# Optimization experiments

Measured on AMD Instinct MI355X. Metric: run time of the kernel, lower is better.

Reference implementation:

```python
import jax, jax.numpy as jnp
import numpy as np

B, L, LOCAL_DIM, M = 4096, 256, 2, 64

def setup_inputs() -> dict:
    key = jax.random.key(0)
    k1, k2 = jax.random.split(key)
    samples = jax.random.randint(k1, (B, L), 0, LOCAL_DIM, dtype=jnp.int32)
    # epsilon near 1 so the product over L=256 sites is numerically stable
    epsilon = 1.0 + 0.05 * jax.random.normal(k2, (LOCAL_DIM, M, L), dtype=jnp.float32)
    return {"samples": samples, "epsilon": epsilon}

def reference(samples, epsilon):
    # samples: (B, L) int occupancies in [0, local_dim)
    # epsilon: (local_dim, M, L)
    # qGPS full path with no_syms: out[b] = sum_m prod_l epsilon[samples[b,l], m, l]
    Ls = samples.shape[-1]
    eps_t = jnp.transpose(epsilon, (2, 0, 1))          # (L, local_dim, M)
    gathered = eps_t[jnp.arange(Ls)[None, :], samples]  # (B, L, M) gather by occupancy
    site_prod = jnp.prod(gathered, axis=1)              # (B, M) product over sites
    return jnp.sum(site_prod, axis=-1)                  # (B,) sum over support dim M
```

## Files before the change

kernel.cpp:

```cpp
#include <hip/hip_runtime.h>

#define LQ 256
#define MQ 64
#define SW 264

typedef __attribute__((ext_vector_type(8))) short bf16x8;
typedef __attribute__((ext_vector_type(4))) float f32x4;

#if defined(__has_builtin) && __has_builtin(__builtin_amdgcn_logf)
#define LOG2F(x) __builtin_amdgcn_logf(x)
#else
#define LOG2F(x) __log2f(x)
#endif
#if defined(__has_builtin) && __has_builtin(__builtin_amdgcn_exp2f)
#define EXP2F(x) __builtin_amdgcn_exp2f(x)
#else
#define EXP2F(x) exp2f(x)
#endif

__device__ __forceinline__ unsigned short f2bf(float x) {
    unsigned u = __float_as_uint(x);
    u += 0x7FFFu + ((u >> 16) & 1u);
    return (unsigned short)(u >> 16);
}

__global__ __launch_bounds__(256) void qgps_mfma(const int* __restrict__ samples,
                                                 const float* __restrict__ eps,
                                                 float* __restrict__ out) {
    __shared__ __attribute__((aligned(16))) unsigned short Wt[MQ * SW];
    __shared__ __attribute__((aligned(16))) unsigned short St[16 * SW];
    __shared__ float bred[MQ * 4];
    __shared__ float red[4][16];

    const int tid = threadIdx.x;
    const int w = tid >> 6;
    const int lane = tid & 63;
    const int b0 = blockIdx.x * 16;

    {
        const int m = tid >> 2;
        const int ls = (tid & 3) * 64;
        const float4* e0v = (const float4*)(eps + m * LQ + ls);
        const float4* e1v = (const float4*)(eps + MQ * LQ + m * LQ + ls);
        unsigned short* wrow = &Wt[m * SW + ls];
        float acc0 = 0.f;
#pragma unroll
        for (int i = 0; i < 16; ++i) {
            float4 a = e0v[i], c = e1v[i];
            float l0 = LOG2F(a.x), l1 = LOG2F(a.y);
            float l2 = LOG2F(a.z), l3 = LOG2F(a.w);
            acc0 += (l0 + l1) + (l2 + l3);
            ushort2 p0 = make_ushort2(f2bf(LOG2F(c.x) - l0), f2bf(LOG2F(c.y) - l1));
            ushort2 p1 = make_ushort2(f2bf(LOG2F(c.z) - l2), f2bf(LOG2F(c.w) - l3));
            *(ushort2*)&wrow[4 * i] = p0;
            *(ushort2*)&wrow[4 * i + 2] = p1;
        }
        bred[m * 4 + (tid & 3)] = acc0;
    }

    {
        const int bl = tid >> 4;
        const int ls = (tid & 15) * 16;
        const int4* sp = (const int4*)(samples + (b0 + bl) * LQ + ls);
        int4 v0 = sp[0], v1 = sp[1], v2 = sp[2], v3 = sp[3];
        bf16x8 o0, o1;
        o0[0] = v0.x ? 0x3F80 : 0; o0[1] = v0.y ? 0x3F80 : 0;
        o0[2] = v0.z ? 0x3F80 : 0; o0[3] = v0.w ? 0x3F80 : 0;
        o0[4] = v1.x ? 0x3F80 : 0; o0[5] = v1.y ? 0x3F80 : 0;
        o0[6] = v1.z ? 0x3F80 : 0; o0[7] = v1.w ? 0x3F80 : 0;
        o1[0] = v2.x ? 0x3F80 : 0; o1[1] = v2.y ? 0x3F80 : 0;
        o1[2] = v2.z ? 0x3F80 : 0; o1[3] = v2.w ? 0x3F80 : 0;
        o1[4] = v3.x ? 0x3F80 : 0; o1[5] = v3.y ? 0x3F80 : 0;
        o1[6] = v3.z ? 0x3F80 : 0; o1[7] = v3.w ? 0x3F80 : 0;
        *(bf16x8*)&St[bl * SW + ls] = o0;
        *(bf16x8*)&St[bl * SW + ls + 8] = o1;
    }
    __syncthreads();

    const int fr = lane & 15;
    const int ko = (lane >> 4) * 8;
    const unsigned short* Ap = &St[fr * SW + ko];
    const unsigned short* Bp = &Wt[(w * 16 + fr) * SW + ko];
    f32x4 acc = {0.f, 0.f, 0.f, 0.f};
#pragma unroll
    for (int k = 0; k < 8; ++k) {
        bf16x8 af = *(const bf16x8*)(Ap + k * 32);
        bf16x8 bf = *(const bf16x8*)(Bp + k * 32);
        acc = __builtin_amdgcn_mfma_f32_16x16x32_bf16(af, bf, acc, 0, 0, 0);
    }

    const int m = w * 16 + fr;
    f32x4 bb = *(f32x4*)&bred[m * 4];
    float base = (bb[0] + bb[1]) + (bb[2] + bb[3]);
    float t0 = EXP2F(base + acc[0]);
    float t1 = EXP2F(base + acc[1]);
    float t2 = EXP2F(base + acc[2]);
    float t3 = EXP2F(base + acc[3]);
#pragma unroll
    for (int off = 1; off < 16; off <<= 1) {
        t0 += __shfl_xor(t0, off, 64);
        t1 += __shfl_xor(t1, off, 64);
        t2 += __shfl_xor(t2, off, 64);
        t3 += __shfl_xor(t3, off, 64);
    }
    if (fr == 0) {
        const int q = lane >> 4;
        red[w][q * 4 + 0] = t0;
        red[w][q * 4 + 1] = t1;
        red[w][q * 4 + 2] = t2;
        red[w][q * 4 + 3] = t3;
    }
    __syncthreads();
    if (tid < 16) {
        float o = (red[0][tid] + red[1][tid]) + (red[2][tid] + red[3][tid]);
        out[b0 + tid] = o;
    }
}

extern "C" void kernel_launch(void* const* d_in, const int* in_sizes, int n_in,
                              void* d_out, int out_size, void* d_ws, size_t ws_size,
                              hipStream_t stream) {
    const int* samples = (const int*)d_in[0];
    const float* eps = (const float*)d_in[1];
    float* out = (float*)d_out;
    (void)d_ws; (void)ws_size;

    qgps_mfma<<<256, 256, 0, stream>>>(samples, eps, out);
}
```

Baseline: 60.69 us.

## Split epsilon log-preprocessing into a prep kernel, load MFMA fragments directly

Moves the log2 transform of epsilon out of each of the 256 main-kernel blocks into a small prep kernel that writes bf16 weights, pre-swizzled in MFMA fragment order, plus per-m base sums to the workspace. The main kernel then loads B fragments straight from global memory and builds A fragments from samples in registers by packing int pairs and multiplying by 0x3F80, removing LDS staging and the first __syncthreads. This removes redundant transcendental work (every block previously recomputed 64x256 logs), at the cost of a second launch and a workspace round trip. The packing trick assumes samples are exactly 0 or 1.

```diff
diff --git a/kernel.cpp b/kernel.cpp
--- a/kernel.cpp
+++ b/kernel.cpp
@@ -1,11 +1,12 @@
 #include <hip/hip_runtime.h>
+
 
 #define LQ 256
 #define MQ 64
-#define SW 264
 
 typedef __attribute__((ext_vector_type(8))) short bf16x8;
 typedef __attribute__((ext_vector_type(4))) float f32x4;
+typedef __attribute__((ext_vector_type(4))) unsigned u32x4;
 
 #if defined(__has_builtin) && __has_builtin(__builtin_amdgcn_logf)
 #define LOG2F(x) __builtin_amdgcn_logf(x)
@@ -24,74 +25,83 @@
     return (unsigned short)(u >> 16);
 }
 
-__global__ __launch_bounds__(256) void qgps_mfma(const int* __restrict__ samples,
-                                                 const float* __restrict__ eps,
+__global__ __launch_bounds__(512) void qgps_prep(const float* __restrict__ eps,
+                                                 unsigned short* __restrict__ Wg,
+                                                 float* __restrict__ baseg) {
+    __shared__ float bred[16][32];
+    const int tid = threadIdx.x;
+    const int k = tid >> 6;
+    const int lane = tid & 63;
+    const int strip = blockIdx.x;
+    const int fr = lane & 15;
+    const int q = lane >> 4;
+    const int m = strip * 16 + fr;
+    const int lb = k * 32 + q * 8;
+
+    const float* e0 = eps + m * LQ + lb;
+    const float* e1 = eps + MQ * LQ + m * LQ + lb;
+    float4 a0 = *(const float4*)e0;
+    float4 a1 = *(const float4*)(e0 + 4);
+    float4 c0 = *(const float4*)e1;
+    float4 c1 = *(const float4*)(e1 + 4);
+
+    float l0 = LOG2F(a0.x), l1 = LOG2F(a0.y), l2 = LOG2F(a0.z), l3 = LOG2F(a0.w);
+    float l4 = LOG2F(a1.x), l5 = LOG2F(a1.y), l6 = LOG2F(a1.z), l7 = LOG2F(a1.w);
+
+    bf16x8 wv;
+    wv[0] = (short)f2bf(LOG2F(c0.x) - l0);
+    wv[1] = (short)f2bf(LOG2F(c0.y) - l1);
+    wv[2] = (short)f2bf(LOG2F(c0.z) - l2);
+    wv[3] = (short)f2bf(LOG2F(c0.w) - l3);
+    wv[4] = (short)f2bf(LOG2F(c1.x) - l4);
+    wv[5] = (short)f2bf(LOG2F(c1.y) - l5);
+    wv[6] = (short)f2bf(LOG2F(c1.z) - l6);
+    wv[7] = (short)f2bf(LOG2F(c1.w) - l7);
+    ((bf16x8*)Wg)[(strip * 8 + k) * 64 + lane] = wv;
+
+    bred[fr][k * 4 + q] = ((l0 + l1) + (l2 + l3)) + ((l4 + l5) + (l6 + l7));
+    __syncthreads();
+    if (tid < 16) {
+        float t = 0.f;
+#pragma unroll
+        for (int i = 0; i < 32; ++i) t += bred[tid][i];
+        baseg[strip * 16 + tid] = t;
+    }
+}
+
+__global__ __launch_bounds__(256) void qgps_main(const int* __restrict__ samples,
+                                                 const unsigned short* __restrict__ Wg,
+                                                 const float* __restrict__ baseg,
                                                  float* __restrict__ out) {
-    __shared__ __attribute__((aligned(16))) unsigned short Wt[MQ * SW];
-    __shared__ __attribute__((aligned(16))) unsigned short St[16 * SW];
-    __shared__ float bred[MQ * 4];
     __shared__ float red[4][16];
-
     const int tid = threadIdx.x;
     const int w = tid >> 6;
     const int lane = tid & 63;
     const int b0 = blockIdx.x * 16;
-
-    {
-        const int m = tid >> 2;
-        const int ls = (tid & 3) * 64;
-        const float4* e0v = (const float4*)(eps + m * LQ + ls);
-        const float4* e1v = (const float4*)(eps + MQ * LQ + m * LQ + ls);
-        unsigned short* wrow = &Wt[m * SW + ls];
-        float acc0 = 0.f;
-#pragma unroll
-        for (int i = 0; i < 16; ++i) {
-            float4 a = e0v[i], c = e1v[i];
-            float l0 = LOG2F(a.x), l1 = LOG2F(a.y);
-            float l2 = LOG2F(a.z), l3 = LOG2F(a.w);
-            acc0 += (l0 + l1) + (l2 + l3);
-            ushort2 p0 = make_ushort2(f2bf(LOG2F(c.x) - l0), f2bf(LOG2F(c.y) - l1));
-            ushort2 p1 = make_ushort2(f2bf(LOG2F(c.z) - l2), f2bf(LOG2F(c.w) - l3));
-            *(ushort2*)&wrow[4 * i] = p0;
-            *(ushort2*)&wrow[4 * i + 2] = p1;
-        }
-        bred[m * 4 + (tid & 3)] = acc0;
-    }
-
-    {
-        const int bl = tid >> 4;
-        const int ls = (tid & 15) * 16;
-        const int4* sp = (const int4*)(samples + (b0 + bl) * LQ + ls);
-        int4 v0 = sp[0], v1 = sp[1], v2 = sp[2], v3 = sp[3];
-        bf16x8 o0, o1;
-        o0[0] = v0.x ? 0x3F80 : 0; o0[1] = v0.y ? 0x3F80 : 0;
-        o0[2] = v0.z ? 0x3F80 : 0; o0[3] = v0.w ? 0x3F80 : 0;
-        o0[4] = v1.x ? 0x3F80 : 0; o0[5] = v1.y ? 0x3F80 : 0;
-        o0[6] = v1.z ? 0x3F80 : 0; o0[7] = v1.w ? 0x3F80 : 0;
-        o1[0] = v2.x ? 0x3F80 : 0; o1[1] = v2.y ? 0x3F80 : 0;
-        o1[2] = v2.z ? 0x3F80 : 0; o1[3] = v2.w ? 0x3F80 : 0;
-        o1[4] = v3.x ? 0x3F80 : 0; o1[5] = v3.y ? 0x3F80 : 0;
-        o1[6] = v3.z ? 0x3F80 : 0; o1[7] = v3.w ? 0x3F80 : 0;
-        *(bf16x8*)&St[bl * SW + ls] = o0;
-        *(bf16x8*)&St[bl * SW + ls + 8] = o1;
-    }
-    __syncthreads();
-
     const int fr = lane & 15;
     const int ko = (lane >> 4) * 8;
-    const unsigned short* Ap = &St[fr * SW + ko];
-    const unsigned short* Bp = &Wt[(w * 16 + fr) * SW + ko];
+
+    const bf16x8* Wv = (const bf16x8*)Wg + w * 8 * 64 + lane;
+    bf16x8 bfr[8];
+#pragma unroll
+    for (int k = 0; k < 8; ++k) bfr[k] = Wv[k * 64];
+
+    const int4* sp = (const int4*)(samples + (b0 + fr) * LQ + ko);
     f32x4 acc = {0.f, 0.f, 0.f, 0.f};
 #pragma unroll
     for (int k = 0; k < 8; ++k) {
-        bf16x8 af = *(const bf16x8*)(Ap + k * 32);
-        bf16x8 bf = *(const bf16x8*)(Bp + k * 32);
-        acc = __builtin_amdgcn_mfma_f32_16x16x32_bf16(af, bf, acc, 0, 0, 0);
+        int4 v0 = sp[k * 8];
+        int4 v1 = sp[k * 8 + 1];
+        u32x4 u;
+        u[0] = (unsigned)((v0.x | (v0.y << 16)) * 0x3F80);
+        u[1] = (unsigned)((v0.z | (v0.w << 16)) * 0x3F80);
+        u[2] = (unsigned)((v1.x | (v1.y << 16)) * 0x3F80);
+        u[3] = (unsigned)((v1.z | (v1.w << 16)) * 0x3F80);
+        acc = __builtin_amdgcn_mfma_f32_16x16x32_bf16(
+            __builtin_bit_cast(bf16x8, u), bfr[k], acc, 0, 0, 0);
     }
 
-    const int m = w * 16 + fr;
-    f32x4 bb = *(f32x4*)&bred[m * 4];
-    float base = (bb[0] + bb[1]) + (bb[2] + bb[3]);
+    const float base = baseg[w * 16 + fr];
     float t0 = EXP2F(base + acc[0]);
     float t1 = EXP2F(base + acc[1]);
     float t2 = EXP2F(base + acc[2]);
@@ -123,7 +133,11 @@
     const int* samples = (const int*)d_in[0];
     const float* eps = (const float*)d_in[1];
     float* out = (float*)d_out;
-    (void)d_ws; (void)ws_size;
 
-    qgps_mfma<<<256, 256, 0, stream>>>(samples, eps, out);
+    unsigned short* Wg = (unsigned short*)d_ws;
+    float* baseg = (float*)((char*)d_ws + 32768);
+    (void)ws_size; (void)in_sizes; (void)n_in; (void)out_size;
+
+    qgps_prep<<<4, 512, 0, stream>>>(eps, Wg, baseg);
+    qgps_main<<<256, 256, 0, stream>>>(samples, Wg, baseg, out);
 }
```

Result: no change. 60.10 us (-1.0%).
